# Kernel optimization log

Hardware: AMD Instinct MI355X
Metric: run time of the kernel (lower is better)

Reference implementation:

```python
import jax, jax.numpy as jnp
import numpy as np

B, T, D, K = 4, 4096, 1024, 8
EPS = 1e-8  # matches torch cosine-similarity norm clamp


def setup_inputs() -> dict:
    key = jax.random.key(0)
    kx, = jax.random.split(key, 1)
    x = jax.random.normal(kx, (B, T, D), dtype=jnp.float32)
    gain = jnp.ones((D,), dtype=jnp.float32)
    bias = jnp.zeros((D,), dtype=jnp.float32)
    log_mix = jnp.zeros((), dtype=jnp.float32)
    log_scale = jnp.zeros((), dtype=jnp.float32)
    return {"x": x, "gain": gain, "bias": bias,
            "log_mix": log_mix, "log_scale": log_scale}


def reference(x, gain, bias, log_mix, log_scale):
    # x: (B, T, D)
    mix = jax.nn.sigmoid(log_mix)
    scale = jax.nn.softplus(log_scale) + 0.01

    # --- causal top-K cosine-similarity adjacency (binary) ---
    xn = x / (jnp.linalg.norm(x, axis=-1, keepdims=True) + EPS)
    sim = jnp.einsum('btd,bsd->bts', xn, xn)              # (B, T, T)
    t = x.shape[1]
    causal = jnp.tril(jnp.ones((t, t), dtype=bool))       # j <= i allowed
    sim = jnp.where(causal[None], sim, -jnp.inf)
    vals, idx = jax.lax.top_k(sim, K)                     # (B, T, K)
    valid = jnp.isfinite(vals)                            # rows i < K have fewer neighbors

    # --- unweighted (mean) neighbor aggregation ---
    gathered = jax.vmap(lambda xb, ib: xb[ib])(x, idx)    # (B, T, K, D)
    cnt = jnp.maximum(valid.sum(-1, keepdims=True), 1).astype(x.dtype)  # (B, T, 1)
    msg = (gathered * valid[..., None].astype(x.dtype)).sum(axis=2) / cnt  # (B, T, D)

    # --- elementwise gate epilogue ---
    blended = mix * x + (1.0 - mix) * msg
    delta = jax.nn.gelu(blended * gain + bias, approximate=False) * scale
    return delta
```

## Files before the change

kernel.cpp:

```cpp
#include <hip/hip_runtime.h>
#include <math.h>

#define B_ 4
#define T_ 4096
#define D_ 1024
#define K_ 8
#define M_ 12

#define NSEG_F16 16
#define NTILE_B  544

#define BI 32
#define BJ 128
#define DC 32

typedef __attribute__((ext_vector_type(8))) _Float16 f16x8;
typedef __attribute__((ext_vector_type(16))) float f32x16;

__device__ __forceinline__ void ins12(float (&tv)[M_], int (&tix)[M_], float v, int nj) {
#pragma unroll
    for (int k = 0; k < M_; ++k) {
        const float nxt = (k < M_ - 1) ? tv[k + 1] : INFINITY;
        const int   nxi = (k < M_ - 1) ? tix[k + 1] : -1;
        const bool  up  = v > nxt;
        const bool  mid = v > tv[k];
        tv[k]  = up ? nxt : (mid ? v  : tv[k]);
        tix[k] = up ? nxi : (mid ? nj : tix[k]);
    }
}

__global__ __launch_bounds__(256) void norm_kernel(const float* __restrict__ x,
                                                   float* __restrict__ rn32,
                                                   double* __restrict__ rn64) {
    const int row = blockIdx.x;
    const int tid = threadIdx.x;
    const float4 v = reinterpret_cast<const float4*>(x + (size_t)row * D_)[tid];
    double ss = (double)v.x * v.x + (double)v.y * v.y +
                (double)v.z * v.z + (double)v.w * v.w;
    for (int o = 32; o > 0; o >>= 1) ss += __shfl_down(ss, o);
    __shared__ double ws[4];
    if ((tid & 63) == 0) ws[tid >> 6] = ss;
    __syncthreads();
    if (tid == 0) {
        double s = ws[0] + ws[1] + ws[2] + ws[3];
        double rn = 1.0 / (sqrt(s) + 1e-8);
        rn64[row] = rn;
        rn32[row] = (float)rn;
    }
}

__global__ __launch_bounds__(256) void pack_transpose_kernel(const float* __restrict__ x,
                                                             const float* __restrict__ rn32,
                                                             _Float16* __restrict__ xf) {
    const int blk = blockIdx.x;
    const int b   = blk >> 6;
    const int i0b = (blk & 63) << 6;
    const int tid = threadIdx.x;
    const int r   = tid >> 2;
    const int q   = tid & 3;
    const int row = i0b + r;
    const float rn = rn32[(b << 12) + row];
    const float* src = x + ((size_t)(b << 12) + row) * D_;
    f16x8* dst = reinterpret_cast<f16x8*>(xf) + (size_t)b * 128 * T_;
#pragma unroll
    for (int g = 0; g < 32; ++g) {
        const int p = (g << 2) + q;
        const float4 a = *reinterpret_cast<const float4*>(src + (p << 3));
        const float4 c = *reinterpret_cast<const float4*>(src + (p << 3) + 4);
        f16x8 h;
        h[0] = (_Float16)(a.x * rn); h[1] = (_Float16)(a.y * rn);
        h[2] = (_Float16)(a.z * rn); h[3] = (_Float16)(a.w * rn);
        h[4] = (_Float16)(c.x * rn); h[5] = (_Float16)(c.y * rn);
        h[6] = (_Float16)(c.z * rn); h[7] = (_Float16)(c.w * rn);
        dst[(size_t)p * T_ + row] = h;
    }
}

__global__ __launch_bounds__(256) void simtopk_f16(const _Float16* __restrict__ xf,
                                                   int* __restrict__ cand_idx,
                                                   float* __restrict__ cand_val) {
    __shared__ float mv[64 * 4 * M_];
    __shared__ int   mi[64 * 4 * M_];

    const int bid = blockIdx.x;
    const int b   = bid / NTILE_B;
    const int u   = bid - b * NTILE_B;
    int q = 0;
#pragma unroll
    for (int qq = 1; qq < 16; ++qq) if (u >= 2 * qq * (qq + 1)) q = qq;
    const int rr = u - 2 * q * (q + 1);
    const int dt = rr / (q + 1);
    const int s  = rr - dt * (q + 1);
    const int t  = (q << 2) + dt;
    const int i0 = t << 6;
    const int j0 = s << 8;

    const int tid  = threadIdx.x;
    const int wid  = tid >> 6;
    const int lane = tid & 63;
    const int l31  = lane & 31;
    const int lhi  = lane >> 5;

    const f16x8* Fb = reinterpret_cast<const f16x8*>(xf) + (size_t)b * 128 * T_;

    const int myc = i0 + (lhi << 5) + l31;
    const int jbw = j0 + (wid << 6);

    float tv[M_]; int tix[M_];
#pragma unroll
    for (int k = 0; k < M_; ++k) { tv[k] = -INFINITY; tix[k] = -1; }

    f32x16 acc00, acc01, acc10, acc11;
#pragma unroll
    for (int r = 0; r < 16; ++r) { acc00[r] = 0.f; acc01[r] = 0.f; acc10[r] = 0.f; acc11[r] = 0.f; }

#pragma unroll 4
    for (int kh = 0; kh < 16; ++kh) {
#pragma unroll
        for (int ks = 0; ks < 4; ++ks) {
            const int p = (kh << 3) + (ks << 1) + lhi;
            const f16x8* Fp = Fb + (size_t)p * T_;
            const f16x8 aj0 = Fp[jbw + l31];
            const f16x8 aj1 = Fp[jbw + 32 + l31];
            const f16x8 bi0 = Fp[i0 + l31];
            const f16x8 bi1 = Fp[i0 + 32 + l31];
            acc00 = __builtin_amdgcn_mfma_f32_32x32x16_f16(aj0, bi0, acc00, 0, 0, 0);
            acc01 = __builtin_amdgcn_mfma_f32_32x32x16_f16(aj0, bi1, acc01, 0, 0, 0);
            acc10 = __builtin_amdgcn_mfma_f32_32x32x16_f16(aj1, bi0, acc10, 0, 0, 0);
            acc11 = __builtin_amdgcn_mfma_f32_32x32x16_f16(aj1, bi1, acc11, 0, 0, 0);
        }
    }

#pragma unroll
    for (int r = 0; r < 16; ++r) {
        const float swA = __shfl_xor(acc00[r], 32);
        const float swB = __shfl_xor(acc01[r], 32);
        const float swC = __shfl_xor(acc10[r], 32);
        const float swD = __shfl_xor(acc11[r], 32);
        const int rbase = (r & 3) + ((r >> 2) << 3);
        const int rown  = jbw + rbase + (lhi << 2);
        const int rotn  = jbw + rbase + ((1 - lhi) << 2);
        const float va = lhi ? acc01[r] : acc00[r];
        const float vb = lhi ? swB      : swA;
        const float vc = lhi ? acc11[r] : acc10[r];
        const float vd = lhi ? swD      : swC;
        if (rown <= myc      && va > tv[0]) ins12(tv, tix, va, rown);
        if (rotn <= myc      && vb > tv[0]) ins12(tv, tix, vb, rotn);
        if (rown + 32 <= myc && vc > tv[0]) ins12(tv, tix, vc, rown + 32);
        if (rotn + 32 <= myc && vd > tv[0]) ins12(tv, tix, vd, rotn + 32);
    }

    const int coll = (lhi << 5) + l31;
#pragma unroll
    for (int k = 0; k < M_; ++k) {
        mv[(coll * 4 + wid) * M_ + k] = tv[k];
        mi[(coll * 4 + wid) * M_ + k] = tix[k];
    }
    __syncthreads();
    if (tid < 64) {
        float gv[M_]; int gx[M_];
#pragma unroll
        for (int k = 0; k < M_; ++k) { gv[k] = -INFINITY; gx[k] = -1; }
        for (int ls = 0; ls < 4; ++ls) {
            const int base = (tid * 4 + ls) * M_;
            for (int k = M_ - 1; k >= 0; --k) {
                const float v = mv[base + k];
                if (!(v > gv[0])) break;
                const int nj = mi[base + k];
                if (nj >= 0) ins12(gv, gx, v, nj);
            }
        }
        const size_t cb = ((size_t)(b * T_ + i0 + tid) * NSEG_F16 + s) * M_;
#pragma unroll
        for (int k = 0; k < M_; ++k) {
            cand_val[cb + k] = gv[M_ - 1 - k];
            cand_idx[cb + k] = gx[M_ - 1 - k];
        }
    }
}

__global__ __launch_bounds__(256) void simtopk_fp32(const float* __restrict__ x,
                                                    const float* __restrict__ rn32,
                                                    int* __restrict__ cand_idx,
                                                    float* __restrict__ cand_val,
                                                    int SEGJT, int NSEGMAX) {
    __shared__ __align__(16) float smem2[DC * 36 + DC * 132];
    float (*At)[36]  = reinterpret_cast<float(*)[36]>(smem2);
    float (*Bt)[132] = reinterpret_cast<float(*)[132]>(smem2 + DC * 36);
    float (*Cs)[132] = reinterpret_cast<float(*)[132]>(smem2);

    const int bid = blockIdx.x;
    const int s   = bid % NSEGMAX;
    const int bt  = bid / NSEGMAX;
    const int t   = bt & 127;
    const int b   = bt >> 7;
    const int njt = (t >> 2) + 1;
    const int jt0 = s * SEGJT;
    if (jt0 >= njt) return;
    const int jt1 = min(jt0 + SEGJT, njt);
    const int i0  = t * BI;

    const int tid = threadIdx.x;
    const int tx  = tid & 31;
    const int ty  = tid >> 5;
    const float* xb = x + (size_t)b * T_ * D_;
    const float* rb = rn32 + b * T_;

    const int ai  = tid >> 3;
    const int adq = (tid & 7) << 2;

    float tv[M_]; int tix[M_];
#pragma unroll
    for (int k = 0; k < M_; ++k) { tv[k] = -INFINITY; tix[k] = -1; }

    for (int jt = jt0; jt < jt1; ++jt) {
        const int j0 = jt << 7;
        float acc[4][4];
#pragma unroll
        for (int ii = 0; ii < 4; ++ii)
#pragma unroll
            for (int jj = 0; jj < 4; ++jj) acc[ii][jj] = 0.f;

        for (int dc = 0; dc < D_; dc += DC) {
            __syncthreads();
            {
                const float rn = rb[i0 + ai];
                float4 v = *reinterpret_cast<const float4*>(&xb[(size_t)(i0 + ai) * D_ + dc + adq]);
                At[adq + 0][ai] = v.x * rn;
                At[adq + 1][ai] = v.y * rn;
                At[adq + 2][ai] = v.z * rn;
                At[adq + 3][ai] = v.w * rn;
            }
#pragma unroll
            for (int l = 0; l < 4; ++l) {
                const int li = tid + (l << 8);
                const int j  = li >> 3;
                const int dq = (li & 7) << 2;
                const float rn = rb[j0 + j];
                float4 v = *reinterpret_cast<const float4*>(&xb[(size_t)(j0 + j) * D_ + dc + dq]);
                Bt[dq + 0][j] = v.x * rn;
                Bt[dq + 1][j] = v.y * rn;
                Bt[dq + 2][j] = v.z * rn;
                Bt[dq + 3][j] = v.w * rn;
            }
            __syncthreads();
#pragma unroll 8
            for (int d = 0; d < DC; ++d) {
                float4 a  = *reinterpret_cast<const float4*>(&At[d][ty << 2]);
                float4 bv = *reinterpret_cast<const float4*>(&Bt[d][tx << 2]);
                float av[4] = {a.x, a.y, a.z, a.w};
                float bw[4] = {bv.x, bv.y, bv.z, bv.w};
#pragma unroll
                for (int ii = 0; ii < 4; ++ii)
#pragma unroll
                    for (int jj = 0; jj < 4; ++jj)
                        acc[ii][jj] = fmaf(av[ii], bw[jj], acc[ii][jj]);
            }
        }
        __syncthreads();
#pragma unroll
        for (int ii = 0; ii < 4; ++ii) {
            *reinterpret_cast<float4*>(&Cs[(ty << 2) + ii][tx << 2]) =
                make_float4(acc[ii][0], acc[ii][1], acc[ii][2], acc[ii][3]);
        }
        __syncthreads();
        if (tid < BI) {
            const int gi   = i0 + tid;
            const int jmax = gi - j0;
            const int cend = jmax < BJ - 1 ? jmax : BJ - 1;
            for (int c = 0; c <= cend; ++c) {
                const float v = Cs[tid][c];
                if (v > tv[0]) ins12(tv, tix, v, j0 + c);
            }
        }
    }
    if (tid < BI) {
        const size_t base = ((size_t)(b * T_ + i0 + tid) * NSEGMAX + s) * M_;
#pragma unroll
        for (int k = 0; k < M_; ++k) {
            cand_idx[base + k] = tix[M_ - 1 - k];
            cand_val[base + k] = tv[M_ - 1 - k];
        }
    }
}

__global__ __launch_bounds__(256) void select_kernel(const float* __restrict__ x,
                                                     const double* __restrict__ rn64,
                                                     const int* __restrict__ cand_idx,
                                                     const float* __restrict__ cand_val,
                                                     int* __restrict__ sel,
                                                     int SEGJT, int NSEGMAX, int SHIFT) {
    const int tid  = threadIdx.x;
    const int wid  = tid >> 6;
    const int lane = tid & 63;
    const int row  = (blockIdx.x << 2) + wid;
    const int b    = row >> 12;
    const int i    = row & (T_ - 1);
    const int njt  = (i >> SHIFT) + 1;
    const int nseg = (njt + SEGJT - 1) / SEGJT;
    const int ncand = nseg * M_;

    __shared__ unsigned long long keys[4][192];
    __shared__ float v12[4][12];
    __shared__ int   i12[4][12];

    if (lane < 12) { v12[wid][lane] = -INFINITY; i12[wid][lane] = -1; }

    const size_t cb = (size_t)row * NSEGMAX * M_;
    float cv[3]; int cj[3]; unsigned long long kk[3];
#pragma unroll
    for (int q = 0; q < 3; ++q) {
        const int c = lane + (q << 6);
        if (c < ncand) { cv[q] = cand_val[cb + c]; cj[q] = cand_idx[cb + c]; }
        else           { cv[q] = -INFINITY;        cj[q] = -1; }
        unsigned u = __float_as_uint(cv[q]);
        unsigned so = (u & 0x80000000u) ? ~u : (u | 0x80000000u);
        kk[q] = (cj[q] >= 0)
              ? ((((unsigned long long)so) << 32) | (unsigned long long)(0xFFFFFFFFu - (unsigned)cj[q]))
              : 0ull;
        keys[wid][lane + (q << 6)] = kk[q];
    }
    int nv = 0;
#pragma unroll
    for (int q = 0; q < 3; ++q) nv += __popcll(__ballot(cj[q] >= 0));
    __syncthreads();

    int rk0 = 0, rk1 = 0, rk2 = 0;
#pragma unroll 4
    for (int c = 0; c < ncand; ++c) {
        const unsigned long long kc = keys[wid][c];
        rk0 += (kc > kk[0]);
        rk1 += (kc > kk[1]);
        rk2 += (kc > kk[2]);
    }
    if (cj[0] >= 0 && rk0 < 12) { v12[wid][rk0] = cv[0]; i12[wid][rk0] = cj[0]; }
    if (cj[1] >= 0 && rk1 < 12) { v12[wid][rk1] = cv[1]; i12[wid][rk1] = cj[1]; }
    if (cj[2] >= 0 && rk2 < 12) { v12[wid][rk2] = cv[2]; i12[wid][rk2] = cj[2]; }
    __syncthreads();

    const float v8 = v12[wid][7];
    const float v9 = v12[wid][8];
    const bool refine = (nv > K_) && (v8 - v9 < 2e-4f);

    int outj = -1;
    int cnt;
    if (refine) {
        const float* xi = x + (size_t)row * D_;
        float4 xa[4];
#pragma unroll
        for (int q = 0; q < 4; ++q)
            xa[q] = *reinterpret_cast<const float4*>(xi + (lane << 4) + (q << 2));
        double sim[12]; int jj[12];
#pragma unroll
        for (int c = 0; c < 12; ++c) {
            const int j = i12[wid][c];
            jj[c] = j;
            double s = 0.0;
            if (j >= 0) {
                const float* xj = x + ((size_t)(b << 12) + j) * D_;
#pragma unroll
                for (int q = 0; q < 4; ++q) {
                    const float4 xc = *reinterpret_cast<const float4*>(xj + (lane << 4) + (q << 2));
                    s += (double)xa[q].x * xc.x + (double)xa[q].y * xc.y +
                         (double)xa[q].z * xc.z + (double)xa[q].w * xc.w;
                }
            }
            sim[c] = s;
        }
#pragma unroll
        for (int c = 0; c < 12; ++c) {
#pragma unroll
            for (int o = 1; o < 64; o <<= 1) sim[c] += __shfl_xor(sim[c], o);
        }
        const double rni = rn64[row];
#pragma unroll
        for (int c = 0; c < 12; ++c)
            sim[c] = (jj[c] >= 0) ? sim[c] * rni * rn64[(b << 12) + jj[c]] : -1e300;
        unsigned msel = 0;
#pragma unroll
        for (int c = 0; c < 12; ++c) {
            int r = 0;
#pragma unroll
            for (int d = 0; d < 12; ++d) {
                if (d == c) continue;
                r += (sim[d] > sim[c]) || (sim[d] == sim[c] && jj[d] < jj[c]);
            }
            if (jj[c] >= 0 && r < 8) msel |= (1u << c);
        }
        cnt = __popc(msel); if (cnt < 1) cnt = 1;
        if (lane < 8) {
            int seen = 0;
#pragma unroll
            for (int c = 0; c < 12; ++c) {
                if (msel & (1u << c)) { if (seen == lane) outj = jj[c]; ++seen; }
            }
        }
    } else {
        cnt = nv < K_ ? nv : K_; if (cnt < 1) cnt = 1;
        if (lane < 8) outj = i12[wid][lane];
    }
    if (lane < 8) sel[(row << 4) + lane] = outj;
    if (lane == 8) sel[(row << 4) + 8] = cnt;
}

__global__ __launch_bounds__(256) void gather_kernel(const float* __restrict__ x,
                                                     const int* __restrict__ sel,
                                                     const float* __restrict__ gain,
                                                     const float* __restrict__ bias,
                                                     const float* __restrict__ lmix,
                                                     const float* __restrict__ lscale,
                                                     float* __restrict__ out) {
    const int row = blockIdx.x;
    const int b   = row >> 12;
    const int tid = threadIdx.x;
    const int sb  = row << 4;

    int js[8];
#pragma unroll
    for (int k = 0; k < 8; ++k) js[k] = sel[sb + k];
    const int cnt = sel[sb + 8];

    const float4 xiv = reinterpret_cast<const float4*>(x + (size_t)row * D_)[tid];
    float mx = 0.f, my = 0.f, mz = 0.f, mw = 0.f;
#pragma unroll
    for (int k = 0; k < 8; ++k) {
        const int j = js[k];
        if (j >= 0) {
            const float4 xc = reinterpret_cast<const float4*>(
                x + ((size_t)(b << 12) + j) * D_)[tid];
            mx += xc.x; my += xc.y; mz += xc.z; mw += xc.w;
        }
    }
    const float inv = 1.0f / (float)cnt;
    const float lm = lmix[0], ls = lscale[0];
    const float mix = 1.0f / (1.0f + expf(-lm));
    const float sc  = (fmaxf(ls, 0.f) + log1pf(expf(-fabsf(ls)))) + 0.01f;
    const float4 g  = reinterpret_cast<const float4*>(gain)[tid];
    const float4 bb = reinterpret_cast<const float4*>(bias)[tid];

    float4 o4;
    {
        float m, bl, y;
        m = mx * inv; bl = mix * xiv.x + (1.f - mix) * m; y = bl * g.x + bb.x;
        o4.x = 0.5f * y * (1.f + erff(y * 0.70710678118654752f)) * sc;
        m = my * inv; bl = mix * xiv.y + (1.f - mix) * m; y = bl * g.y + bb.y;
        o4.y = 0.5f * y * (1.f + erff(y * 0.70710678118654752f)) * sc;
        m = mz * inv; bl = mix * xiv.z + (1.f - mix) * m; y = bl * g.z + bb.z;
        o4.z = 0.5f * y * (1.f + erff(y * 0.70710678118654752f)) * sc;
        m = mw * inv; bl = mix * xiv.w + (1.f - mix) * m; y = bl * g.w + bb.w;
        o4.w = 0.5f * y * (1.f + erff(y * 0.70710678118654752f)) * sc;
    }
    reinterpret_cast<float4*>(out + (size_t)row * D_)[tid] = o4;
}

extern "C" void kernel_launch(void* const* d_in, const int* in_sizes, int n_in,
                              void* d_out, int out_size, void* d_ws, size_t ws_size,
                              hipStream_t stream) {
    const float* x      = (const float*)d_in[0];
    const float* gain   = (const float*)d_in[1];
    const float* bias   = (const float*)d_in[2];
    const float* lmix   = (const float*)d_in[3];
    const float* lscale = (const float*)d_in[4];
    float* out = (float*)d_out;

    char* ws = (char*)d_ws;
    float*  rn32 = (float*)ws;
    double* rn64 = (double*)(ws + 65536);
    int*    selb = (int*)(ws + 196608);
    const size_t base2 = 196608 + (size_t)B_ * T_ * 16 * 4;
    const size_t HF = (size_t)B_ * T_ * D_ * 2;
    _Float16* xf = (_Float16*)(ws + base2);
    const size_t base_cand = base2 + HF;

    auto candBytes = [](int nseg) { return (size_t)B_ * T_ * nseg * M_ * 8; };

    const bool use_f16 = (ws_size >= base_cand + candBytes(NSEG_F16));

    if (use_f16) {
        int*   cidx = (int*)(ws + base_cand);
        float* cval = (float*)(ws + base_cand + candBytes(NSEG_F16) / 2);
        norm_kernel<<<dim3(B_ * T_), dim3(256), 0, stream>>>(x, rn32, rn64);
        pack_transpose_kernel<<<dim3(B_ * T_ / 64), dim3(256), 0, stream>>>(x, rn32, xf);
        simtopk_f16<<<dim3(B_ * NTILE_B), dim3(256), 0, stream>>>(xf, cidx, cval);
        select_kernel<<<dim3(B_ * T_ / 4), dim3(256), 0, stream>>>(
            x, rn64, cidx, cval, selb, 1, NSEG_F16, 8);
    } else {
        int SEG2, NSEG2;
        if (ws_size >= base2 + candBytes(9)) { SEG2 = 4;  NSEG2 = 9; }
        else                                 { SEG2 = 33; NSEG2 = 1; }
        int*   cidx = (int*)(ws + base2);
        float* cval = (float*)(ws + base2 + candBytes(NSEG2) / 2);
        norm_kernel<<<dim3(B_ * T_), dim3(256), 0, stream>>>(x, rn32, rn64);
        simtopk_fp32<<<dim3(B_ * 128 * NSEG2), dim3(256), 0, stream>>>(x, rn32, cidx, cval, SEG2, NSEG2);
        select_kernel<<<dim3(B_ * T_ / 4), dim3(256), 0, stream>>>(
            x, rn64, cidx, cval, selb, SEG2, NSEG2, 7);
    }
    gather_kernel<<<dim3(B_ * T_), dim3(256), 0, stream>>>(
        x, selb, gain, bias, lmix, lscale, out);
}
```

Baseline: 320.6 us.

## Software-pipeline f16 similarity MFMA loads and reorder tile schedule by column segment

Replaces the unrolled load-then-MFMA loop with an explicit double-buffered register pipeline that issues the next group's global loads before the current group's MFMAs, so memory latency is hidden behind matrix work. It also changes the block-to-tile mapping so blocks iterate column segment first instead of the triangular row-group order, which alters cache locality between concurrently scheduled blocks. Doubling the live operand registers raises register pressure and may cut occupancy.

```diff
diff --git a/kernel.cpp b/kernel.cpp
--- a/kernel.cpp
+++ b/kernel.cpp
@@ -85,13 +85,10 @@
     const int bid = blockIdx.x;
     const int b   = bid / NTILE_B;
     const int u   = bid - b * NTILE_B;
-    int q = 0;
-#pragma unroll
-    for (int qq = 1; qq < 16; ++qq) if (u >= 2 * qq * (qq + 1)) q = qq;
-    const int rr = u - 2 * q * (q + 1);
-    const int dt = rr / (q + 1);
-    const int s  = rr - dt * (q + 1);
-    const int t  = (q << 2) + dt;
+    int s = 0;
+#pragma unroll
+    for (int ss = 1; ss < 16; ++ss) if (u >= ss * (66 - 2 * ss)) s = ss;
+    const int t  = (s << 2) + (u - s * (66 - 2 * s));
     const int i0 = t << 6;
     const int j0 = s << 8;
 
@@ -106,31 +103,46 @@
     const int myc = i0 + (lhi << 5) + l31;
     const int jbw = j0 + (wid << 6);
 
+    const f16x8* Jb = Fb + jbw + l31;
+    const f16x8* Ib = Fb + i0  + l31;
+
+    f32x16 acc00, acc01, acc10, acc11;
+#pragma unroll
+    for (int r = 0; r < 16; ++r) { acc00[r] = 0.f; acc01[r] = 0.f; acc10[r] = 0.f; acc11[r] = 0.f; }
+
+    f16x8 ca0, ca1, ca2, ca3, cb0, cb1, cb2, cb3;
+    f16x8 na0, na1, na2, na3, nb0, nb1, nb2, nb3;
+    {
+        const size_t p0 = (size_t)lhi * T_;
+        const size_t p1 = (size_t)(2 + lhi) * T_;
+        ca0 = Jb[p0]; ca1 = Jb[p0 + 32]; cb0 = Ib[p0]; cb1 = Ib[p0 + 32];
+        ca2 = Jb[p1]; ca3 = Jb[p1 + 32]; cb2 = Ib[p1]; cb3 = Ib[p1 + 32];
+    }
+#pragma unroll
+    for (int g = 0; g < 32; ++g) {
+        if (g < 31) {
+            const size_t p0 = (size_t)((g << 2) + 4 + lhi) * T_;
+            const size_t p1 = (size_t)((g << 2) + 6 + lhi) * T_;
+            na0 = Jb[p0]; na1 = Jb[p0 + 32]; nb0 = Ib[p0]; nb1 = Ib[p0 + 32];
+            na2 = Jb[p1]; na3 = Jb[p1 + 32]; nb2 = Ib[p1]; nb3 = Ib[p1 + 32];
+        }
+        acc00 = __builtin_amdgcn_mfma_f32_32x32x16_f16(ca0, cb0, acc00, 0, 0, 0);
+        acc01 = __builtin_amdgcn_mfma_f32_32x32x16_f16(ca0, cb1, acc01, 0, 0, 0);
+        acc10 = __builtin_amdgcn_mfma_f32_32x32x16_f16(ca1, cb0, acc10, 0, 0, 0);
+        acc11 = __builtin_amdgcn_mfma_f32_32x32x16_f16(ca1, cb1, acc11, 0, 0, 0);
+        acc00 = __builtin_amdgcn_mfma_f32_32x32x16_f16(ca2, cb2, acc00, 0, 0, 0);
+        acc01 = __builtin_amdgcn_mfma_f32_32x32x16_f16(ca2, cb3, acc01, 0, 0, 0);
+        acc10 = __builtin_amdgcn_mfma_f32_32x32x16_f16(ca3, cb2, acc10, 0, 0, 0);
+        acc11 = __builtin_amdgcn_mfma_f32_32x32x16_f16(ca3, cb3, acc11, 0, 0, 0);
+        if (g < 31) {
+            ca0 = na0; ca1 = na1; ca2 = na2; ca3 = na3;
+            cb0 = nb0; cb1 = nb1; cb2 = nb2; cb3 = nb3;
+        }
+    }
+
     float tv[M_]; int tix[M_];
 #pragma unroll
     for (int k = 0; k < M_; ++k) { tv[k] = -INFINITY; tix[k] = -1; }
-
-    f32x16 acc00, acc01, acc10, acc11;
-#pragma unroll
-    for (int r = 0; r < 16; ++r) { acc00[r] = 0.f; acc01[r] = 0.f; acc10[r] = 0.f; acc11[r] = 0.f; }
-
-#pragma unroll 4
-    for (int kh = 0; kh < 16; ++kh) {
-#pragma unroll
-        for (int ks = 0; ks < 4; ++ks) {
-            const int p = (kh << 3) + (ks << 1) + lhi;
-            const f16x8* Fp = Fb + (size_t)p * T_;
-            const f16x8 aj0 = Fp[jbw + l31];
-            const f16x8 aj1 = Fp[jbw + 32 + l31];
-            const f16x8 bi0 = Fp[i0 + l31];
-            const f16x8 bi1 = Fp[i0 + 32 + l31];
-            acc00 = __builtin_amdgcn_mfma_f32_32x32x16_f16(aj0, bi0, acc00, 0, 0, 0);
-            acc01 = __builtin_amdgcn_mfma_f32_32x32x16_f16(aj0, bi1, acc01, 0, 0, 0);
-            acc10 = __builtin_amdgcn_mfma_f32_32x32x16_f16(aj1, bi0, acc10, 0, 0, 0);
-            acc11 = __builtin_amdgcn_mfma_f32_32x32x16_f16(aj1, bi1, acc11, 0, 0, 0);
-        }
-    }
-
 #pragma unroll
     for (int r = 0; r < 16; ++r) {
         const float swA = __shfl_xor(acc00[r], 32);
```

Result: slower. 367.2 us (+14.6%).

## Widen similarity tile to 128 query rows per block for operand reuse

Applied to the files above, without the earlier changes.

Each block of the fused similarity/top-k kernel now covers 128 query rows instead of 64. Each wave holds eight MFMA accumulators rather than four, so every key-row fragment load feeds twice as many MFMAs. The triangular tile enumeration is recomputed for the halved tile count, and the candidate scan and merge are run for both 64-row halves. The cost is twice the accumulator registers and LDS, which may lower occupancy, and coarser diagonal tiles that do more wasted causal work.

```diff
diff --git a/kernel.cpp b/kernel.cpp
--- a/kernel.cpp
+++ b/kernel.cpp
@@ -8,7 +8,7 @@
 #define M_ 12
 
 #define NSEG_F16 16
-#define NTILE_B  544
+#define NTILE_B  272
 
 #define BI 32
 #define BJ 128
@@ -26,6 +26,30 @@
         const bool  mid = v > tv[k];
         tv[k]  = up ? nxt : (mid ? v  : tv[k]);
         tix[k] = up ? nxi : (mid ? nj : tix[k]);
+    }
+}
+
+__device__ __forceinline__ void scan_cons(const f32x16& c00, const f32x16& c01,
+                                          const f32x16& c10, const f32x16& c11,
+                                          int jbw, int lhi, int myc,
+                                          float (&tv)[M_], int (&tix)[M_]) {
+#pragma unroll
+    for (int r = 0; r < 16; ++r) {
+        const float swA = __shfl_xor(c00[r], 32);
+        const float swB = __shfl_xor(c01[r], 32);
+        const float swC = __shfl_xor(c10[r], 32);
+        const float swD = __shfl_xor(c11[r], 32);
+        const int rbase = (r & 3) + ((r >> 2) << 3);
+        const int rown  = jbw + rbase + (lhi << 2);
+        const int rotn  = jbw + rbase + ((1 - lhi) << 2);
+        const float va = lhi ? c01[r] : c00[r];
+        const float vb = lhi ? swB    : swA;
+        const float vc = lhi ? c11[r] : c10[r];
+        const float vd = lhi ? swD    : swC;
+        if (rown <= myc      && va > tv[0]) ins12(tv, tix, va, rown);
+        if (rotn <= myc      && vb > tv[0]) ins12(tv, tix, vb, rotn);
+        if (rown + 32 <= myc && vc > tv[0]) ins12(tv, tix, vc, rown + 32);
+        if (rotn + 32 <= myc && vd > tv[0]) ins12(tv, tix, vd, rotn + 32);
     }
 }
 
@@ -79,20 +103,20 @@
 __global__ __launch_bounds__(256) void simtopk_f16(const _Float16* __restrict__ xf,
                                                    int* __restrict__ cand_idx,
                                                    float* __restrict__ cand_val) {
-    __shared__ float mv[64 * 4 * M_];
-    __shared__ int   mi[64 * 4 * M_];
+    __shared__ float mv[128 * 4 * M_];
+    __shared__ int   mi[128 * 4 * M_];
 
     const int bid = blockIdx.x;
     const int b   = bid / NTILE_B;
     const int u   = bid - b * NTILE_B;
     int q = 0;
 #pragma unroll
-    for (int qq = 1; qq < 16; ++qq) if (u >= 2 * qq * (qq + 1)) q = qq;
-    const int rr = u - 2 * q * (q + 1);
+    for (int qq = 1; qq < 16; ++qq) if (u >= qq * (qq + 1)) q = qq;
+    const int rr = u - q * (q + 1);
     const int dt = rr / (q + 1);
     const int s  = rr - dt * (q + 1);
-    const int t  = (q << 2) + dt;
-    const int i0 = t << 6;
+    const int t  = (q << 1) + dt;
+    const int i0 = t << 7;
     const int j0 = s << 8;
 
     const int tid  = threadIdx.x;
@@ -103,16 +127,16 @@
 
     const f16x8* Fb = reinterpret_cast<const f16x8*>(xf) + (size_t)b * 128 * T_;
 
-    const int myc = i0 + (lhi << 5) + l31;
     const int jbw = j0 + (wid << 6);
-
-    float tv[M_]; int tix[M_];
-#pragma unroll
-    for (int k = 0; k < M_; ++k) { tv[k] = -INFINITY; tix[k] = -1; }
-
-    f32x16 acc00, acc01, acc10, acc11;
-#pragma unroll
-    for (int r = 0; r < 16; ++r) { acc00[r] = 0.f; acc01[r] = 0.f; acc10[r] = 0.f; acc11[r] = 0.f; }
+    const int mycA = i0 + (lhi << 5) + l31;
+    const int mycB = mycA + 64;
+
+    f32x16 a00, a01, a02, a03, a10, a11, a12, a13;
+#pragma unroll
+    for (int r = 0; r < 16; ++r) {
+        a00[r] = 0.f; a01[r] = 0.f; a02[r] = 0.f; a03[r] = 0.f;
+        a10[r] = 0.f; a11[r] = 0.f; a12[r] = 0.f; a13[r] = 0.f;
+    }
 
 #pragma unroll 4
     for (int kh = 0; kh < 16; ++kh) {
@@ -124,40 +148,45 @@
             const f16x8 aj1 = Fp[jbw + 32 + l31];
             const f16x8 bi0 = Fp[i0 + l31];
             const f16x8 bi1 = Fp[i0 + 32 + l31];
-            acc00 = __builtin_amdgcn_mfma_f32_32x32x16_f16(aj0, bi0, acc00, 0, 0, 0);
-            acc01 = __builtin_amdgcn_mfma_f32_32x32x16_f16(aj0, bi1, acc01, 0, 0, 0);
-            acc10 = __builtin_amdgcn_mfma_f32_32x32x16_f16(aj1, bi0, acc10, 0, 0, 0);
-            acc11 = __builtin_amdgcn_mfma_f32_32x32x16_f16(aj1, bi1, acc11, 0, 0, 0);
-        }
-    }
-
-#pragma unroll
-    for (int r = 0; r < 16; ++r) {
-        const float swA = __shfl_xor(acc00[r], 32);
-        const float swB = __shfl_xor(acc01[r], 32);
-        const float swC = __shfl_xor(acc10[r], 32);
-        const float swD = __shfl_xor(acc11[r], 32);
-        const int rbase = (r & 3) + ((r >> 2) << 3);
-        const int rown  = jbw + rbase + (lhi << 2);
-        const int rotn  = jbw + rbase + ((1 - lhi) << 2);
-        const float va = lhi ? acc01[r] : acc00[r];
-        const float vb = lhi ? swB      : swA;
-        const float vc = lhi ? acc11[r] : acc10[r];
-        const float vd = lhi ? swD      : swC;
-        if (rown <= myc      && va > tv[0]) ins12(tv, tix, va, rown);
-        if (rotn <= myc      && vb > tv[0]) ins12(tv, tix, vb, rotn);
-        if (rown + 32 <= myc && vc > tv[0]) ins12(tv, tix, vc, rown + 32);
-        if (rotn + 32 <= myc && vd > tv[0]) ins12(tv, tix, vd, rotn + 32);
-    }
-
-    const int coll = (lhi << 5) + l31;
-#pragma unroll
-    for (int k = 0; k < M_; ++k) {
-        mv[(coll * 4 + wid) * M_ + k] = tv[k];
-        mi[(coll * 4 + wid) * M_ + k] = tix[k];
+            const f16x8 bi2 = Fp[i0 + 64 + l31];
+            const f16x8 bi3 = Fp[i0 + 96 + l31];
+            a00 = __builtin_amdgcn_mfma_f32_32x32x16_f16(aj0, bi0, a00, 0, 0, 0);
+            a01 = __builtin_amdgcn_mfma_f32_32x32x16_f16(aj0, bi1, a01, 0, 0, 0);
+            a02 = __builtin_amdgcn_mfma_f32_32x32x16_f16(aj0, bi2, a02, 0, 0, 0);
+            a03 = __builtin_amdgcn_mfma_f32_32x32x16_f16(aj0, bi3, a03, 0, 0, 0);
+            a10 = __builtin_amdgcn_mfma_f32_32x32x16_f16(aj1, bi0, a10, 0, 0, 0);
+            a11 = __builtin_amdgcn_mfma_f32_32x32x16_f16(aj1, bi1, a11, 0, 0, 0);
+            a12 = __builtin_amdgcn_mfma_f32_32x32x16_f16(aj1, bi2, a12, 0, 0, 0);
+            a13 = __builtin_amdgcn_mfma_f32_32x32x16_f16(aj1, bi3, a13, 0, 0, 0);
+        }
+    }
+
+    {
+        float tv[M_]; int tix[M_];
+#pragma unroll
+        for (int k = 0; k < M_; ++k) { tv[k] = -INFINITY; tix[k] = -1; }
+        scan_cons(a00, a01, a10, a11, jbw, lhi, mycA, tv, tix);
+        const int colA = (lhi << 5) + l31;
+#pragma unroll
+        for (int k = 0; k < M_; ++k) {
+            mv[(colA * 4 + wid) * M_ + k] = tv[k];
+            mi[(colA * 4 + wid) * M_ + k] = tix[k];
+        }
+    }
+    {
+        float tv[M_]; int tix[M_];
+#pragma unroll
+        for (int k = 0; k < M_; ++k) { tv[k] = -INFINITY; tix[k] = -1; }
+        scan_cons(a02, a03, a12, a13, jbw, lhi, mycB, tv, tix);
+        const int colB = 64 + (lhi << 5) + l31;
+#pragma unroll
+        for (int k = 0; k < M_; ++k) {
+            mv[(colB * 4 + wid) * M_ + k] = tv[k];
+            mi[(colB * 4 + wid) * M_ + k] = tix[k];
+        }
     }
     __syncthreads();
-    if (tid < 64) {
+    if (tid < 128) {
         float gv[M_]; int gx[M_];
 #pragma unroll
         for (int k = 0; k < M_; ++k) { gv[k] = -INFINITY; gx[k] = -1; }
```

Result: slower. 825.5 us (+157.5%).
